# Performance work log

Hardware: AMD Instinct MI355X
Metric: run time of the kernel (lower is better)

The kernel has to match this reference:

```python
import jax, jax.numpy as jnp
import numpy as np

D_MODEL, H, D_FF = 512, 8, 2048
DK = D_MODEL // H
EPS = 1e-5  # torch LayerNorm default


def layer_norm(x, g, b):
    m = jnp.mean(x, axis=-1, keepdims=True)
    v = jnp.mean((x - m) ** 2, axis=-1, keepdims=True)
    return (x - m) * jax.lax.rsqrt(v + EPS) * g + b


def setup_inputs() -> dict:
    key = jax.random.key(0)
    ks = jax.random.split(key, 10)
    B, S = 8, 2048
    s = lambda fan_in: 1.0 / np.sqrt(fan_in)
    return {
        "x": jax.random.normal(ks[0], (B, S, D_MODEL), jnp.float32),
        # per-head projections stacked: [h, d_model, dk] (bias-free Project)
        "wq": jax.random.uniform(ks[1], (H, D_MODEL, DK), jnp.float32, -s(D_MODEL), s(D_MODEL)),
        "wk": jax.random.uniform(ks[2], (H, D_MODEL, DK), jnp.float32, -s(D_MODEL), s(D_MODEL)),
        "wv": jax.random.uniform(ks[3], (H, D_MODEL, DK), jnp.float32, -s(D_MODEL), s(D_MODEL)),
        "wo": jax.random.uniform(ks[4], (D_MODEL, D_MODEL), jnp.float32, -s(D_MODEL), s(D_MODEL)),
        "w1": jax.random.uniform(ks[5], (D_MODEL, D_FF), jnp.float32, -s(D_MODEL), s(D_MODEL)),
        "b1": jax.random.uniform(ks[6], (D_FF,), jnp.float32, -s(D_MODEL), s(D_MODEL)),
        "w2": jax.random.uniform(ks[7], (D_FF, D_MODEL), jnp.float32, -s(D_FF), s(D_FF)),
        "b2": jax.random.uniform(ks[8], (D_MODEL,), jnp.float32, -s(D_FF), s(D_FF)),
        "ln1_g": jnp.ones((D_MODEL,), jnp.float32),
        "ln1_b": jnp.zeros((D_MODEL,), jnp.float32),
        "ln2_g": jnp.ones((D_MODEL,), jnp.float32),
        "ln2_b": jnp.zeros((D_MODEL,), jnp.float32),
    }


def reference(x, wq, wk, wv, wo, w1, b1, w2, b2, ln1_g, ln1_b, ln2_g, ln2_b):
    B, S, D = x.shape
    # --- multi-head self-attention (8 per-head Linears fused into one einsum) ---
    q = jnp.einsum("bsd,hdk->bhsk", x, wq)
    k = jnp.einsum("bsd,hdk->bhsk", x, wk)
    v = jnp.einsum("bsd,hdk->bhsk", x, wv)
    score = jnp.einsum("bhsk,bhtk->bhst", q, k) * (1.0 / np.sqrt(DK))
    attn = jax.nn.softmax(score, axis=-1)
    heads = jnp.einsum("bhst,bhtk->bhsk", attn, v)
    concat = heads.transpose(0, 2, 1, 3).reshape(B, S, D)  # cat over heads
    mha = concat @ wo
    # dropout in eval mode -> identity
    x = layer_norm(mha + x, ln1_g, ln1_b)
    # --- feed-forward ---
    ffn = jax.nn.relu(x @ w1 + b1) @ w2 + b2
    return layer_norm(ffn + x, ln2_g, ln2_b)
```

## Files before the change

### kernel.cpp

```cpp
#include <hip/hip_runtime.h>
#include <hip/hip_bf16.h>
#include <math.h>


#define D_MODEL 512
#define NHEAD   8
#define DKH     64
#define SEQ     2048
#define BATCH   8
#define DFF     2048
#define MROWS   (BATCH * SEQ)
#define QKVLD   1536

typedef __bf16 bf16x8 __attribute__((ext_vector_type(8)));
typedef float  f32x4  __attribute__((ext_vector_type(4)));

__device__ __forceinline__ unsigned short f2bf(float f) {
    union { float f; unsigned u; } v; v.f = f;
    return (unsigned short)((v.u + 0x7FFFu + ((v.u >> 16) & 1u)) >> 16);
}

__device__ __forceinline__ float bf2f(unsigned short u) {
    union { unsigned u; float f; } v; v.u = (unsigned)u << 16;
    return v.f;
}

__device__ __forceinline__ unsigned cvtpk(float a, float b) {
    unsigned r;
    asm("v_cvt_pk_bf16_f32 %0, %1, %2" : "=v"(r) : "v"(a), "v"(b));
    return r;
}

__device__ __forceinline__ float fexp2(float x) {
    float r; asm("v_exp_f32 %0, %1" : "=v"(r) : "v"(x)); return r;
}

__device__ __forceinline__ f32x4 mfma16(bf16x8 a, bf16x8 b, f32x4 c) {
    return __builtin_amdgcn_mfma_f32_16x16x32_bf16(a, b, c, 0, 0, 0);
}

__device__ __forceinline__ void gld_lds16(const unsigned short* g, unsigned short* l) {
    __builtin_amdgcn_global_load_lds(
        (const __attribute__((address_space(1))) unsigned int*)g,
        (__attribute__((address_space(3))) unsigned int*)l, 16, 0, 0);
}

template<bool BIAS, bool RELU, int RESMODE, bool OUTF32>
__global__ __launch_bounds__(256)
void mfma_gemm(const unsigned short* __restrict__ Av,
               const unsigned short* __restrict__ Bt,
               const float* __restrict__ bias, const void* __restrict__ resv,
               void* __restrict__ Cv, int Kdim, int lda, int ldc)
{
    __shared__ unsigned short As[2][128][32];
    __shared__ unsigned short Bs[2][128][32];

    const int tid  = threadIdx.x;
    const int lane = tid & 63;
    const int w    = tid >> 6;
    const int mq   = (w >> 1) << 6;
    const int nq   = (w & 1) << 6;
    const int lrow = lane & 15;
    const int g    = lane >> 4;
    const int lk   = g << 3;

    const int row0 = blockIdx.y << 7;
    const int col0 = blockIdx.x << 7;

    const int c0   = w << 5;
    const int srow = lane >> 2;
    const int scol = (lane & 3) << 3;
    const size_t aoff = (size_t)(row0 + c0 + srow) * lda  + scol;
    const size_t boff = (size_t)(col0 + c0 + srow) * Kdim + scol;

    auto stage = [&](int buf, int kt) {
        gld_lds16(Av + aoff + kt,                        &As[buf][c0     ][0]);
        gld_lds16(Av + aoff + (size_t)16 * lda  + kt,    &As[buf][c0 + 16][0]);
        gld_lds16(Bt + boff + kt,                        &Bs[buf][c0     ][0]);
        gld_lds16(Bt + boff + (size_t)16 * Kdim + kt,    &Bs[buf][c0 + 16][0]);
    };

    const f32x4 zero = {0.f, 0.f, 0.f, 0.f};
    f32x4 acc[4][4];
    #pragma unroll
    for (int i = 0; i < 4; ++i)
        #pragma unroll
        for (int j = 0; j < 4; ++j) acc[i][j] = zero;

    stage(0, 0);
    __syncthreads();

    int cur = 0;
    for (int kt = 0; kt < Kdim; kt += 32) {
        if (kt + 32 < Kdim) stage(cur ^ 1, kt + 32);

        bf16x8 af[4], bfv[4];
        #pragma unroll
        for (int mf = 0; mf < 4; ++mf)
            af[mf] = *(const bf16x8*)&As[cur][mq + mf * 16 + lrow][lk];
        #pragma unroll
        for (int nf = 0; nf < 4; ++nf)
            bfv[nf] = *(const bf16x8*)&Bs[cur][nq + nf * 16 + lrow][lk];
        #pragma unroll
        for (int mf = 0; mf < 4; ++mf)
            #pragma unroll
            for (int nf = 0; nf < 4; ++nf)
                acc[mf][nf] = mfma16(af[mf], bfv[nf], acc[mf][nf]);

        __syncthreads();
        cur ^= 1;
    }

    const int orow = row0 + mq + g * 4;
    const int ocol = col0 + nq + lrow;
    #pragma unroll
    for (int mf = 0; mf < 4; ++mf) {
        #pragma unroll
        for (int nf = 0; nf < 4; ++nf) {
            const int cc = ocol + nf * 16;
            float bv = 0.f;
            if constexpr (BIAS) bv = bias[cc];
            float v[4];
            #pragma unroll
            for (int r = 0; r < 4; ++r) {
                const int rr = orow + mf * 16 + r;
                v[r] = acc[mf][nf][r];
                if constexpr (BIAS) v[r] += bv;
                if constexpr (RELU) v[r] = fmaxf(v[r], 0.f);
                if constexpr (RESMODE == 1)
                    v[r] += ((const float*)resv)[(size_t)rr * ldc + cc];
                if constexpr (RESMODE == 2)
                    v[r] += bf2f(((const unsigned short*)resv)[(size_t)rr * ldc + cc]);
                if constexpr (OUTF32) ((float*)Cv)[(size_t)rr * ldc + cc] = v[r];
            }
            if constexpr (!OUTF32) {
                const unsigned u01 = cvtpk(v[0], v[1]);
                const unsigned u23 = cvtpk(v[2], v[3]);
                unsigned short* cp = (unsigned short*)Cv + (size_t)(orow + mf * 16) * ldc + cc;
                cp[0]                 = (unsigned short)u01;
                cp[(size_t)ldc]       = (unsigned short)(u01 >> 16);
                cp[(size_t)ldc * 2]   = (unsigned short)u23;
                cp[(size_t)ldc * 3]   = (unsigned short)(u23 >> 16);
            }
        }
    }
}

__device__ __forceinline__ void softmax_store(
    f32x4* sacc, float* mrun, float* lpart, f32x4* oacc,
    unsigned short (*Ps)[76], int rowbase, int g, int lrow)
{
    float pmax[4];
    bool need = false;
    #pragma unroll
    for (int r = 0; r < 4; ++r) {
        pmax[r] = fmaxf(fmaxf(sacc[0][r], sacc[1][r]),
                        fmaxf(sacc[2][r], sacc[3][r]));
        need |= (pmax[r] > mrun[r] + 8.f);
    }
    if (__any(need)) {
        #pragma unroll
        for (int r = 0; r < 4; ++r) {
            float mt = pmax[r];
            mt = fmaxf(mt, __shfl_xor(mt, 1, 16));
            mt = fmaxf(mt, __shfl_xor(mt, 2, 16));
            mt = fmaxf(mt, __shfl_xor(mt, 4, 16));
            mt = fmaxf(mt, __shfl_xor(mt, 8, 16));
            const float mnew = fmaxf(mrun[r], mt);
            const float alpha = fexp2(mrun[r] - mnew);
            mrun[r] = mnew;
            lpart[r] *= alpha;
            #pragma unroll
            for (int nf = 0; nf < 4; ++nf) oacc[nf][r] *= alpha;
        }
    }
    #pragma unroll
    for (int r = 0; r < 4; ++r) {
        const float p0 = fexp2(sacc[0][r] - mrun[r]);
        const float p1 = fexp2(sacc[1][r] - mrun[r]);
        const float p2 = fexp2(sacc[2][r] - mrun[r]);
        const float p3 = fexp2(sacc[3][r] - mrun[r]);
        lpart[r] += (p0 + p1) + (p2 + p3);
        uint2 u;
        u.x = cvtpk(p0, p1);
        u.y = cvtpk(p2, p3);
        *(uint2*)&Ps[rowbase + g * 4 + r][4 * lrow] = u;
    }
}

__global__ __launch_bounds__(512, 4)
void mfma_attn(unsigned short* __restrict__ qkv)
{
    __shared__ unsigned short Ks[64][72];
    __shared__ unsigned short Vt[64][72];
    __shared__ unsigned short Ps[256][76];

    const int tid  = threadIdx.x;
    const int lane = tid & 63;
    const int w    = tid >> 6;
    const int lrow = lane & 15;
    const int g    = lane >> 4;
    const int lk   = g << 3;

    const int bid  = blockIdx.x;
    const int idx  = bid >> 3;
    const int bh   = (bid & 7) * 8 + (idx & 7);
    const int b  = bh >> 3, h = bh & 7;
    const int s0 = (idx >> 3) << 8;

    unsigned short* qptr = qkv + ((size_t)(b * SEQ + s0)) * QKVLD + h * DKH;
    const unsigned short* kbase = qkv + ((size_t)(b * SEQ)) * QKVLD + 512 + h * DKH;
    const unsigned short* vbase = qkv + ((size_t)(b * SEQ)) * QKVLD + 1024 + h * DKH;

    bf16x8 qf[2][2];
    #pragma unroll
    for (int sub = 0; sub < 2; ++sub) {
        const unsigned short* qp = qptr + (size_t)(w * 32 + sub * 16 + lrow) * QKVLD;
        qf[sub][0] = *(const bf16x8*)(qp + lk);
        qf[sub][1] = *(const bf16x8*)(qp + 32 + lk);
    }

    const int kr = tid >> 3, kc = (tid & 7) << 3;
    const int vr = tid & 63, vc = (tid >> 6) << 3;
    const int cvr = ((vr & 15) << 2) | (vr >> 4);

    uint4 kreg, vreg;
    auto loadKV = [&](int t0) {
        kreg = *(const uint4*)(kbase + (size_t)(t0 + kr) * QKVLD + kc);
        vreg = *(const uint4*)(vbase + (size_t)(t0 + vr) * QKVLD + vc);
    };
    loadKV(0);

    const f32x4 zero = {0.f, 0.f, 0.f, 0.f};
    f32x4 oacc0[4], oacc1[4];
    float m0[4], l0[4], m1[4], l1[4];
    #pragma unroll
    for (int i = 0; i < 4; ++i) {
        oacc0[i] = zero; oacc1[i] = zero;
        m0[i] = -INFINITY; m1[i] = -INFINITY; l0[i] = 0.f; l1[i] = 0.f;
    }

    for (int t0 = 0; t0 < SEQ; t0 += 64) {
        __syncthreads();
        *(uint4*)&Ks[kr][kc] = kreg;
        {
            const unsigned short* vu = (const unsigned short*)&vreg;
            #pragma unroll
            for (int j = 0; j < 8; ++j) Vt[vc + j][cvr] = vu[j];
        }
        __syncthreads();

        if (t0 + 64 < SEQ) loadKV(t0 + 64);

        f32x4 s0a[4], s1a[4];
        #pragma unroll
        for (int nf = 0; nf < 4; ++nf) { s0a[nf] = zero; s1a[nf] = zero; }
        __builtin_amdgcn_s_setprio(1);
        #pragma unroll
        for (int kk = 0; kk < 2; ++kk) {
            #pragma unroll
            for (int nf = 0; nf < 4; ++nf) {
                const bf16x8 kf = *(const bf16x8*)&Ks[nf * 16 + lrow][kk * 32 + lk];
                s0a[nf] = mfma16(qf[0][kk], kf, s0a[nf]);
                s1a[nf] = mfma16(qf[1][kk], kf, s1a[nf]);
            }
        }
        __builtin_amdgcn_s_setprio(0);

        softmax_store(s0a, m0, l0, oacc0, Ps, w * 32,      g, lrow);
        softmax_store(s1a, m1, l1, oacc1, Ps, w * 32 + 16, g, lrow);

        __builtin_amdgcn_s_setprio(1);
        #pragma unroll
        for (int kk = 0; kk < 2; ++kk) {
            const bf16x8 pf0 = *(const bf16x8*)&Ps[w * 32 + lrow][kk * 32 + lk];
            const bf16x8 pf1 = *(const bf16x8*)&Ps[w * 32 + 16 + lrow][kk * 32 + lk];
            #pragma unroll
            for (int nf = 0; nf < 4; ++nf) {
                const bf16x8 vf = *(const bf16x8*)&Vt[nf * 16 + lrow][kk * 32 + lk];
                oacc0[nf] = mfma16(pf0, vf, oacc0[nf]);
                oacc1[nf] = mfma16(pf1, vf, oacc1[nf]);
            }
        }
        __builtin_amdgcn_s_setprio(0);
    }

    #pragma unroll
    for (int r = 0; r < 4; ++r) {
        float l = l0[r];
        l += __shfl_xor(l, 1, 16);
        l += __shfl_xor(l, 2, 16);
        l += __shfl_xor(l, 4, 16);
        l += __shfl_xor(l, 8, 16);
        const float inv = 1.f / l;
        #pragma unroll
        for (int nf = 0; nf < 4; ++nf)
            qptr[(size_t)(w * 32 + g * 4 + r) * QKVLD + nf * 16 + lrow] =
                f2bf(oacc0[nf][r] * inv);
    }
    #pragma unroll
    for (int r = 0; r < 4; ++r) {
        float l = l1[r];
        l += __shfl_xor(l, 1, 16);
        l += __shfl_xor(l, 2, 16);
        l += __shfl_xor(l, 4, 16);
        l += __shfl_xor(l, 8, 16);
        const float inv = 1.f / l;
        #pragma unroll
        for (int nf = 0; nf < 4; ++nf)
            qptr[(size_t)(w * 32 + 16 + g * 4 + r) * QKVLD + nf * 16 + lrow] =
                f2bf(oacc1[nf][r] * inv);
    }
}

template<bool WF32, bool WB16>
__global__ __launch_bounds__(256)
void ln_kernel(const float* __restrict__ in, const float* __restrict__ gg,
               const float* __restrict__ bb, float* __restrict__ outf,
               unsigned short* __restrict__ outb)
{
    const int row = blockIdx.x * 4 + (threadIdx.x >> 6);
    const int lane = threadIdx.x & 63;
    const float* p = in + (size_t)row * D_MODEL;

    const float4 a = *(const float4*)(p + lane * 4);
    const float4 c = *(const float4*)(p + 256 + lane * 4);
    float sum = a.x + a.y + a.z + a.w + c.x + c.y + c.z + c.w;
    float sq  = a.x*a.x + a.y*a.y + a.z*a.z + a.w*a.w
              + c.x*c.x + c.y*c.y + c.z*c.z + c.w*c.w;
    #pragma unroll
    for (int msk = 1; msk < 64; msk <<= 1) {
        sum += __shfl_xor(sum, msk, 64);
        sq  += __shfl_xor(sq,  msk, 64);
    }
    const float mean = sum * (1.f / 512.f);
    const float var  = sq * (1.f / 512.f) - mean * mean;
    const float rs   = rsqrtf(var + 1e-5f);

    const float4 g0 = *(const float4*)(gg + lane * 4);
    const float4 g1 = *(const float4*)(gg + 256 + lane * 4);
    const float4 b0 = *(const float4*)(bb + lane * 4);
    const float4 b1 = *(const float4*)(bb + 256 + lane * 4);

    float4 o0, o1;
    o0.x = (a.x - mean) * rs * g0.x + b0.x;
    o0.y = (a.y - mean) * rs * g0.y + b0.y;
    o0.z = (a.z - mean) * rs * g0.z + b0.z;
    o0.w = (a.w - mean) * rs * g0.w + b0.w;
    o1.x = (c.x - mean) * rs * g1.x + b1.x;
    o1.y = (c.y - mean) * rs * g1.y + b1.y;
    o1.z = (c.z - mean) * rs * g1.z + b1.z;
    o1.w = (c.w - mean) * rs * g1.w + b1.w;
    if constexpr (WF32) {
        *(float4*)(outf + (size_t)row * D_MODEL + lane * 4) = o0;
        *(float4*)(outf + (size_t)row * D_MODEL + 256 + lane * 4) = o1;
    }
    if constexpr (WB16) {
        uint2 pa, pb;
        pa.x = cvtpk(o0.x, o0.y);
        pa.y = cvtpk(o0.z, o0.w);
        pb.x = cvtpk(o1.x, o1.y);
        pb.y = cvtpk(o1.z, o1.w);
        *(uint2*)(outb + (size_t)row * D_MODEL + lane * 4) = pa;
        *(uint2*)(outb + (size_t)row * D_MODEL + 256 + lane * 4) = pb;
    }
}

__global__ __launch_bounds__(256)
void cast_bf16(const float* __restrict__ in, unsigned short* __restrict__ out)
{
    const size_t i = ((size_t)blockIdx.x * 256 + threadIdx.x) * 8;
    const float4 a = *(const float4*)(in + i);
    const float4 b = *(const float4*)(in + i + 4);
    uint4 o;
    o.x = cvtpk(a.x, a.y);
    o.y = cvtpk(a.z, a.w);
    o.z = cvtpk(b.x, b.y);
    o.w = cvtpk(b.z, b.w);
    *(uint4*)(out + i) = o;
}

__global__ __launch_bounds__(256)
void pack_qkv(const float* __restrict__ wq, const float* __restrict__ wk,
              const float* __restrict__ wv, unsigned short* __restrict__ Wqkv)
{
    const int idx = blockIdx.x * 256 + threadIdx.x;
    const int n = idx >> 9, d = idx & 511;
    const int h = n >> 6, c = n & 63;
    const size_t src = ((size_t)h * 512 + d) * 64 + c;
    Wqkv[idx]                 = f2bf(wq[src] * 0.18033688f);
    Wqkv[idx + 512 * 512]     = f2bf(wk[src]);
    Wqkv[idx + 2 * 512 * 512] = f2bf(wv[src]);
}

__global__ __launch_bounds__(256)
void pack_t(const float* __restrict__ in, unsigned short* __restrict__ out,
            int K, int N)
{
    __shared__ float t[32][33];
    const int kb = blockIdx.x << 5, nb = blockIdx.y << 5;
    const int c = threadIdx.x & 31, r0 = threadIdx.x >> 5;
    #pragma unroll
    for (int j = 0; j < 32; j += 8)
        t[r0 + j][c] = in[(size_t)(kb + r0 + j) * N + nb + c];
    __syncthreads();
    #pragma unroll
    for (int j = 0; j < 32; j += 8)
        out[(size_t)(nb + r0 + j) * K + kb + c] = f2bf(t[c][r0 + j]);
}

extern "C" void kernel_launch(void* const* d_in, const int* in_sizes, int n_in,
                              void* d_out, int out_size, void* d_ws, size_t ws_size,
                              hipStream_t stream)
{
    (void)in_sizes; (void)n_in; (void)out_size;

    const float* x    = (const float*)d_in[0];
    const float* wq   = (const float*)d_in[1];
    const float* wk   = (const float*)d_in[2];
    const float* wv   = (const float*)d_in[3];
    const float* wo   = (const float*)d_in[4];
    const float* w1   = (const float*)d_in[5];
    const float* b1   = (const float*)d_in[6];
    const float* w2   = (const float*)d_in[7];
    const float* b2   = (const float*)d_in[8];
    const float* ln1g = (const float*)d_in[9];
    const float* ln1b = (const float*)d_in[10];
    const float* ln2g = (const float*)d_in[11];
    const float* ln2b = (const float*)d_in[12];
    float* out = (float*)d_out;

    const size_t QKV_BYTES = (size_t)MROWS * QKVLD * 2;
    const size_t Y_BYTES   = (size_t)MROWS * D_MODEL * 4;
    unsigned char* base = (unsigned char*)d_ws;
    unsigned short* qkv  = (unsigned short*)(base);
    float*          y    = (float*)(base + QKV_BYTES);
    unsigned short* Wqkv = (unsigned short*)(base + QKV_BYTES + Y_BYTES);
    unsigned short* wo_t = Wqkv + 3 * 512 * 512;
    unsigned short* w1_t = wo_t + 512 * 512;
    unsigned short* w2_t = w1_t + 2048 * 512;
    unsigned short* hid  = w2_t + 2048 * 512;

    const size_t hid_off = (size_t)((unsigned char*)hid - base);
    const size_t avail = (ws_size > hid_off) ? (ws_size - hid_off) : 0;
    int chunk = (int)(avail / ((size_t)DFF * 2));
    chunk &= ~127;
    if (chunk > MROWS) chunk = MROWS;
    if (chunk < 128)   chunk = 128;

    float* y2 = (float*)qkv;
    unsigned short* xb  = (unsigned short*)d_out;
    unsigned short* x1b = (unsigned short*)d_out;

    pack_qkv<<<1024, 256, 0, stream>>>(wq, wk, wv, Wqkv);
    pack_t<<<dim3(16, 16), 256, 0, stream>>>(wo, wo_t, 512, 512);
    pack_t<<<dim3(16, 64), 256, 0, stream>>>(w1, w1_t, 512, 2048);
    pack_t<<<dim3(64, 16), 256, 0, stream>>>(w2, w2_t, 2048, 512);
    cast_bf16<<<(MROWS * D_MODEL) / (256 * 8), 256, 0, stream>>>(x, xb);

    const dim3 blk(256);

    mfma_gemm<false, false, 0, false>
        <<<dim3(12, MROWS / 128), blk, 0, stream>>>(xb, Wqkv, nullptr, nullptr,
                                                    qkv, 512, 512, QKVLD);

    mfma_attn<<<dim3(512), dim3(512), 0, stream>>>(qkv);

    mfma_gemm<false, false, 1, true>
        <<<dim3(4, MROWS / 128), blk, 0, stream>>>(qkv, wo_t, nullptr, x, y,
                                                   512, QKVLD, 512);

    ln_kernel<false, true><<<MROWS / 4, blk, 0, stream>>>(y, ln1g, ln1b,
                                                          nullptr, x1b);

    for (int r0 = 0; r0 < MROWS; r0 += chunk) {
        const int rows = (r0 + chunk <= MROWS) ? chunk : (MROWS - r0);
        mfma_gemm<true, true, 0, false>
            <<<dim3(DFF / 128, rows / 128), blk, 0, stream>>>(
                x1b + (size_t)r0 * D_MODEL, w1_t, b1, nullptr, hid,
                512, 512, DFF);
        mfma_gemm<true, false, 2, true>
            <<<dim3(4, rows / 128), blk, 0, stream>>>(
                hid, w2_t, b2, x1b + (size_t)r0 * D_MODEL,
                y2 + (size_t)r0 * D_MODEL, DFF, DFF, 512);
    }

    ln_kernel<true, false><<<MROWS / 4, blk, 0, stream>>>(y2, ln2g, ln2b,
                                                          out, nullptr);
}
```

Baseline: 297.3 us.

## Enlarge attention query tile to 512 rows and double-buffer K/V in LDS

Each attention block now processes 512 query rows, with 64 rows per wave split into four 16-row subtiles, instead of 256. K fragments are loaded once per key tile into registers and reused across all four subtiles, and V fragments are reused across subtiles in the PV product. K/V LDS tiles are double-buffered, which removes one __syncthreads per iteration, and the grid is halved to 256 blocks. The trade-off is higher register pressure (launch bounds drop to 2 blocks per CU) and fewer resident waves for hiding latency.

```diff
diff --git a/kernel.cpp b/kernel.cpp
--- a/kernel.cpp
+++ b/kernel.cpp
@@ -188,12 +188,12 @@
     }
 }
 
-__global__ __launch_bounds__(512, 4)
+__global__ __launch_bounds__(512, 2)
 void mfma_attn(unsigned short* __restrict__ qkv)
 {
-    __shared__ unsigned short Ks[64][72];
-    __shared__ unsigned short Vt[64][72];
-    __shared__ unsigned short Ps[256][76];
+    __shared__ unsigned short Ks[2][64][72];
+    __shared__ unsigned short Vt[2][64][72];
+    __shared__ unsigned short Ps[512][76];
 
     const int tid  = threadIdx.x;
     const int lane = tid & 63;
@@ -206,16 +206,16 @@
     const int idx  = bid >> 3;
     const int bh   = (bid & 7) * 8 + (idx & 7);
     const int b  = bh >> 3, h = bh & 7;
-    const int s0 = (idx >> 3) << 8;
+    const int s0 = (idx >> 3) << 9;
 
     unsigned short* qptr = qkv + ((size_t)(b * SEQ + s0)) * QKVLD + h * DKH;
     const unsigned short* kbase = qkv + ((size_t)(b * SEQ)) * QKVLD + 512 + h * DKH;
     const unsigned short* vbase = qkv + ((size_t)(b * SEQ)) * QKVLD + 1024 + h * DKH;
 
-    bf16x8 qf[2][2];
-    #pragma unroll
-    for (int sub = 0; sub < 2; ++sub) {
-        const unsigned short* qp = qptr + (size_t)(w * 32 + sub * 16 + lrow) * QKVLD;
+    bf16x8 qf[4][2];
+    #pragma unroll
+    for (int sub = 0; sub < 4; ++sub) {
+        const unsigned short* qp = qptr + (size_t)(w * 64 + sub * 16 + lrow) * QKVLD;
         qf[sub][0] = *(const bf16x8*)(qp + lk);
         qf[sub][1] = *(const bf16x8*)(qp + 32 + lk);
     }
@@ -232,84 +232,84 @@
     loadKV(0);
 
     const f32x4 zero = {0.f, 0.f, 0.f, 0.f};
-    f32x4 oacc0[4], oacc1[4];
-    float m0[4], l0[4], m1[4], l1[4];
-    #pragma unroll
-    for (int i = 0; i < 4; ++i) {
-        oacc0[i] = zero; oacc1[i] = zero;
-        m0[i] = -INFINITY; m1[i] = -INFINITY; l0[i] = 0.f; l1[i] = 0.f;
-    }
+    f32x4 oacc[4][4];
+    float m[4][4], l[4][4];
+    #pragma unroll
+    for (int s = 0; s < 4; ++s)
+        #pragma unroll
+        for (int i = 0; i < 4; ++i) {
+            oacc[s][i] = zero; m[s][i] = -INFINITY; l[s][i] = 0.f;
+        }
 
     for (int t0 = 0; t0 < SEQ; t0 += 64) {
-        __syncthreads();
-        *(uint4*)&Ks[kr][kc] = kreg;
+        const int cur = (t0 >> 6) & 1;
+        *(uint4*)&Ks[cur][kr][kc] = kreg;
         {
             const unsigned short* vu = (const unsigned short*)&vreg;
             #pragma unroll
-            for (int j = 0; j < 8; ++j) Vt[vc + j][cvr] = vu[j];
+            for (int j = 0; j < 8; ++j) Vt[cur][vc + j][cvr] = vu[j];
         }
         __syncthreads();
 
         if (t0 + 64 < SEQ) loadKV(t0 + 64);
 
-        f32x4 s0a[4], s1a[4];
-        #pragma unroll
-        for (int nf = 0; nf < 4; ++nf) { s0a[nf] = zero; s1a[nf] = zero; }
+        bf16x8 kf[2][4];
+        #pragma unroll
+        for (int kk = 0; kk < 2; ++kk)
+            #pragma unroll
+            for (int nf = 0; nf < 4; ++nf)
+                kf[kk][nf] = *(const bf16x8*)&Ks[cur][nf * 16 + lrow][kk * 32 + lk];
+
+        #pragma unroll
+        for (int sub = 0; sub < 4; ++sub) {
+            f32x4 sacc[4];
+            #pragma unroll
+            for (int nf = 0; nf < 4; ++nf) sacc[nf] = zero;
+            __builtin_amdgcn_s_setprio(1);
+            #pragma unroll
+            for (int kk = 0; kk < 2; ++kk)
+                #pragma unroll
+                for (int nf = 0; nf < 4; ++nf)
+                    sacc[nf] = mfma16(qf[sub][kk], kf[kk][nf], sacc[nf]);
+            __builtin_amdgcn_s_setprio(0);
+            softmax_store(sacc, m[sub], l[sub], oacc[sub], Ps,
+                          w * 64 + sub * 16, g, lrow);
+        }
+
         __builtin_amdgcn_s_setprio(1);
         #pragma unroll
         for (int kk = 0; kk < 2; ++kk) {
-            #pragma unroll
-            for (int nf = 0; nf < 4; ++nf) {
-                const bf16x8 kf = *(const bf16x8*)&Ks[nf * 16 + lrow][kk * 32 + lk];
-                s0a[nf] = mfma16(qf[0][kk], kf, s0a[nf]);
-                s1a[nf] = mfma16(qf[1][kk], kf, s1a[nf]);
+            bf16x8 vf[4];
+            #pragma unroll
+            for (int nf = 0; nf < 4; ++nf)
+                vf[nf] = *(const bf16x8*)&Vt[cur][nf * 16 + lrow][kk * 32 + lk];
+            #pragma unroll
+            for (int sub = 0; sub < 4; ++sub) {
+                const bf16x8 pf =
+                    *(const bf16x8*)&Ps[w * 64 + sub * 16 + lrow][kk * 32 + lk];
+                #pragma unroll
+                for (int nf = 0; nf < 4; ++nf)
+                    oacc[sub][nf] = mfma16(pf, vf[nf], oacc[sub][nf]);
             }
         }
         __builtin_amdgcn_s_setprio(0);
-
-        softmax_store(s0a, m0, l0, oacc0, Ps, w * 32,      g, lrow);
-        softmax_store(s1a, m1, l1, oacc1, Ps, w * 32 + 16, g, lrow);
-
-        __builtin_amdgcn_s_setprio(1);
-        #pragma unroll
-        for (int kk = 0; kk < 2; ++kk) {
-            const bf16x8 pf0 = *(const bf16x8*)&Ps[w * 32 + lrow][kk * 32 + lk];
-            const bf16x8 pf1 = *(const bf16x8*)&Ps[w * 32 + 16 + lrow][kk * 32 + lk];
-            #pragma unroll
-            for (int nf = 0; nf < 4; ++nf) {
-                const bf16x8 vf = *(const bf16x8*)&Vt[nf * 16 + lrow][kk * 32 + lk];
-                oacc0[nf] = mfma16(pf0, vf, oacc0[nf]);
-                oacc1[nf] = mfma16(pf1, vf, oacc1[nf]);
-            }
-        }
-        __builtin_amdgcn_s_setprio(0);
-    }
-
-    #pragma unroll
-    for (int r = 0; r < 4; ++r) {
-        float l = l0[r];
-        l += __shfl_xor(l, 1, 16);
-        l += __shfl_xor(l, 2, 16);
-        l += __shfl_xor(l, 4, 16);
-        l += __shfl_xor(l, 8, 16);
-        const float inv = 1.f / l;
-        #pragma unroll
-        for (int nf = 0; nf < 4; ++nf)
-            qptr[(size_t)(w * 32 + g * 4 + r) * QKVLD + nf * 16 + lrow] =
-                f2bf(oacc0[nf][r] * inv);
-    }
-    #pragma unroll
-    for (int r = 0; r < 4; ++r) {
-        float l = l1[r];
-        l += __shfl_xor(l, 1, 16);
-        l += __shfl_xor(l, 2, 16);
-        l += __shfl_xor(l, 4, 16);
-        l += __shfl_xor(l, 8, 16);
-        const float inv = 1.f / l;
-        #pragma unroll
-        for (int nf = 0; nf < 4; ++nf)
-            qptr[(size_t)(w * 32 + 16 + g * 4 + r) * QKVLD + nf * 16 + lrow] =
-                f2bf(oacc1[nf][r] * inv);
+    }
+
+    #pragma unroll
+    for (int sub = 0; sub < 4; ++sub) {
+        #pragma unroll
+        for (int r = 0; r < 4; ++r) {
+            float lv = l[sub][r];
+            lv += __shfl_xor(lv, 1, 16);
+            lv += __shfl_xor(lv, 2, 16);
+            lv += __shfl_xor(lv, 4, 16);
+            lv += __shfl_xor(lv, 8, 16);
+            const float inv = 1.f / lv;
+            #pragma unroll
+            for (int nf = 0; nf < 4; ++nf)
+                qptr[(size_t)(w * 64 + sub * 16 + g * 4 + r) * QKVLD
+                     + nf * 16 + lrow] = f2bf(oacc[sub][nf][r] * inv);
+        }
     }
 }
 
@@ -464,7 +464,7 @@
         <<<dim3(12, MROWS / 128), blk, 0, stream>>>(xb, Wqkv, nullptr, nullptr,
                                                     qkv, 512, 512, QKVLD);
 
-    mfma_attn<<<dim3(512), dim3(512), 0, stream>>>(qkv);
+    mfma_attn<<<dim3(256), dim3(512), 0, stream>>>(qkv);
 
     mfma_gemm<false, false, 1, true>
         <<<dim3(4, MROWS / 128), blk, 0, stream>>>(qkv, wo_t, nullptr, x, y,
```

Result: no change. 300.5 us (+1.1%).
